# Kernel optimization log

Hardware: AMD Instinct MI355X
Metric: run time of the kernel (lower is better)

## Reference

```python
import jax, jax.numpy as jnp
import numpy as np

N = 50000        # nodes
E = 800000       # edges
D_IN = 128       # input feature dim
HID = 64         # hidden_dim
HEADS = 4
OUT = 2          # output_dim (fraud / not-fraud)
BN_EPS = 1e-5
NEG_SLOPE = 0.2  # PyG GATv2Conv default


def setup_inputs() -> dict:
    key = jax.random.key(0)
    ks = jax.random.split(key, 16)
    g = lambda k, shape, s=0.05: (jax.random.normal(k, shape, jnp.float32) * s)
    HC = HEADS * HID  # 256
    return {
        "x": jax.random.normal(ks[0], (N, D_IN), jnp.float32),
        "edge_index": jax.random.randint(ks[1], (2, E), 0, N),
        # input projection
        "W_in": g(ks[2], (D_IN, HID)), "b_in": jnp.zeros((HID,), jnp.float32),
        # GATv2 layer 0: HID -> HID, 4 heads (concat -> 256)
        "Wl0": g(ks[3], (HID, HC)), "Wr0": g(ks[4], (HID, HC)),
        "att0": g(ks[5], (HEADS, HID)), "bias0": jnp.zeros((HC,), jnp.float32),
        # GATv2 layer 1: 256 -> HID, 4 heads (concat -> 256)
        "Wl1": g(ks[6], (HC, HC)), "Wr1": g(ks[7], (HC, HC)),
        "att1": g(ks[8], (HEADS, HID)), "bias1": jnp.zeros((HC,), jnp.float32),
        # GATv2 layer 2: 256 -> OUT, 1 head
        "Wl2": g(ks[9], (HC, OUT)), "Wr2": g(ks[10], (HC, OUT)),
        "att2": g(ks[11], (1, OUT)), "bias2": jnp.zeros((OUT,), jnp.float32),
        # BatchNorm (eval mode: running stats) for the first num_layers-1 = 2 layers
        "bn_gamma": jnp.ones((2, HC), jnp.float32),
        "bn_beta": jnp.zeros((2, HC), jnp.float32),
        "bn_mean": jnp.zeros((2, HC), jnp.float32),
        "bn_var": jnp.ones((2, HC), jnp.float32),
    }


def _gatv2(h, src, dst, Wl, Wr, att, bias):
    """PyG GATv2Conv (concat=True, negative_slope=0.2). src->dst messages."""
    n = h.shape[0]
    heads, c = att.shape
    xl = (h @ Wl).reshape(n, heads, c)   # source transform
    xr = (h @ Wr).reshape(n, heads, c)   # target transform
    e = jax.nn.leaky_relu(xl[src] + xr[dst], NEG_SLOPE)       # [E, H, C]
    logits = jnp.einsum('ehc,hc->eh', e, att)                 # [E, H]
    # segment softmax over incoming edges of each destination node
    m = jax.ops.segment_max(logits, dst, num_segments=n)      # [N, H]
    ex = jnp.exp(logits - m[dst])
    denom = jax.ops.segment_sum(ex, dst, num_segments=n)
    alpha = ex / denom[dst]                                   # [E, H]
    out = jax.ops.segment_sum(xl[src] * alpha[..., None], dst, num_segments=n)
    return out.reshape(n, heads * c) + bias


def _bn_eval(h, gamma, beta, mean, var):
    return gamma * (h - mean) * jax.lax.rsqrt(var + BN_EPS) + beta


def reference(x, edge_index, W_in, b_in, Wl0, Wr0, att0, bias0,
              Wl1, Wr1, att1, bias1, Wl2, Wr2, att2, bias2,
              bn_gamma, bn_beta, bn_mean, bn_var):
    n = x.shape[0]
    loop = jnp.arange(n)
    src = jnp.concatenate([edge_index[0], loop])  # PyG add_self_loops=True
    dst = jnp.concatenate([edge_index[1], loop])

    h = jax.nn.relu(x @ W_in + b_in)              # dropout is identity in eval

    # layer 0 (no residual: 64 != 256)
    h = _gatv2(h, src, dst, Wl0, Wr0, att0, bias0)
    h = jax.nn.relu(_bn_eval(h, bn_gamma[0], bn_beta[0], bn_mean[0], bn_var[0]))

    # layer 1 (residual: 256 == 256)
    h_prev = h
    h = _gatv2(h, src, dst, Wl1, Wr1, att1, bias1)
    h = jax.nn.relu(_bn_eval(h, bn_gamma[1], bn_beta[1], bn_mean[1], bn_var[1]))
    h = h + h_prev

    # output layer, 1 head
    h = _gatv2(h, src, dst, Wl2, Wr2, att2, bias2)
    return jax.nn.log_softmax(h, axis=1)
```

## Files before the change

### kernel.cpp

```cpp
#include <hip/hip_runtime.h>
#include <hip/hip_bf16.h>
#include <math.h>


using h16     = _Float16;
using half2v  = __attribute__((ext_vector_type(2))) h16;
using half4v  = __attribute__((ext_vector_type(4))) h16;
using half8   = __attribute__((ext_vector_type(8))) h16;
using floatx2 = __attribute__((ext_vector_type(2))) float;
using floatx4 = __attribute__((ext_vector_type(4))) float;

__device__ __forceinline__ float lrelu(float x) { return x > 0.f ? x : 0.2f * x; }

__device__ __forceinline__ half2v shfl_xor_h2(half2v v, int mask) {
    float f = __builtin_bit_cast(float, v);
    f = __shfl_xor(f, mask, 64);
    return __builtin_bit_cast(half2v, f);
}

__global__ __launch_bounds__(256) void scan_blk(const int* __restrict__ deg,
                                                int* __restrict__ rowstart,
                                                int* __restrict__ bsum,
                                                int* __restrict__ bins, int N) {
    __shared__ int lhist[32];
    if (threadIdx.x < 32) lhist[threadIdx.x] = 0;
    __syncthreads();
    int t = blockIdx.x * 256 + threadIdx.x;
    int lane = threadIdx.x & 63, wid = threadIdx.x >> 6;
    int v = 0;
    if (t < N) {
        v = (deg[t] + 4) & ~3;
        atomicAdd(&lhist[min(v >> 2, 31)], 1);
    }
    int x = v;
#pragma unroll
    for (int off = 1; off < 64; off <<= 1) {
        int y = __shfl_up(x, off, 64);
        if (lane >= off) x += y;
    }
    __shared__ int wsum[4];
    if (lane == 63) wsum[wid] = x;
    __syncthreads();
    int add = 0;
#pragma unroll
    for (int w = 0; w < 4; ++w) if (w < wid) add += wsum[w];
    int incl = x + add;
    if (t < N) rowstart[t] = incl - v;
    if (threadIdx.x == 255) bsum[blockIdx.x] = incl;
    if (threadIdx.x < 32) {
        int c = lhist[threadIdx.x];
        if (c) atomicAdd(&bins[threadIdx.x], c);
    }
}

__global__ __launch_bounds__(256) void scan_off(int* __restrict__ bsum, int NB,
                                                const int* __restrict__ bins,
                                                int* __restrict__ bincur) {
    int t = threadIdx.x;
    int lane = t & 63, wid = t >> 6;
    int v = (t < NB) ? bsum[t] : 0;
    int x = v;
#pragma unroll
    for (int off = 1; off < 64; off <<= 1) {
        int y = __shfl_up(x, off, 64);
        if (lane >= off) x += y;
    }
    __shared__ int wsum[4];
    if (lane == 63) wsum[wid] = x;
    __syncthreads();
    int add = 0;
#pragma unroll
    for (int w = 0; w < 4; ++w) if (w < wid) add += wsum[w];
    if (t < NB) bsum[t] = x + add - v;
    if (t < 32) {
        int b = bins[t];
        int xb = b;
#pragma unroll
        for (int off2 = 1; off2 < 32; off2 <<= 1) {
            int y = __shfl_up(xb, off2, 64);
            if (t >= off2) xb += y;
        }
        bincur[t] = xb - b;
    }
}

__global__ __launch_bounds__(256) void add_off(
        const int* __restrict__ bsum, const int* __restrict__ deg,
        int* __restrict__ rowstart, int* __restrict__ cursor,
        int* __restrict__ csr_src,
        int* __restrict__ bincur, int* __restrict__ perm, int N) {
    __shared__ int lhist[32], lbase[32], lcur[32];
    if (threadIdx.x < 32) { lhist[threadIdx.x] = 0; lcur[threadIdx.x] = 0; }
    __syncthreads();
    int t = blockIdx.x * 256 + threadIdx.x;
    int b = 0;
    bool valid = t < N;
    if (valid) {
        int r = rowstart[t] + bsum[blockIdx.x];
        rowstart[t] = r;
        cursor[t] = r;
        int dg = deg[t];
        int npad = (dg + 4) & ~3;
        for (int k = dg; k < npad; ++k) csr_src[r + k] = t;
        b = min(npad >> 2, 31);
        atomicAdd(&lhist[b], 1);
    }
    __syncthreads();
    if (threadIdx.x < 32) {
        int c = lhist[threadIdx.x];
        lbase[threadIdx.x] = c ? atomicAdd(&bincur[threadIdx.x], c) : 0;
    }
    __syncthreads();
    if (valid) {
        int rank = atomicAdd(&lcur[b], 1);
        perm[lbase[b] + rank] = t;
    }
}

__device__ __forceinline__ void pack_one(const float* __restrict__ W,
                                         h16* __restrict__ Wp,
                                         int t, int K, int NC) {
    int j = t & 7;
    int l = (t >> 3) & 63;
    int rest = t >> 9;
    int NT = NC >> 4;
    int nt = rest % NT;
    int kc = rest / NT;
    int row = kc * 32 + (l >> 4) * 8 + j;
    int col = nt * 16 + (l & 15);
    Wp[t] = (h16)W[(size_t)row * NC + col];
}

__global__ void pack_all(const float* __restrict__ W_in,
                         const float* __restrict__ Wl0, const float* __restrict__ Wr0,
                         const float* __restrict__ Wl1, const float* __restrict__ Wr1,
                         h16* __restrict__ P_in,
                         h16* __restrict__ P_l0, h16* __restrict__ P_r0,
                         h16* __restrict__ P_l1, h16* __restrict__ P_r1,
                         const float4* __restrict__ x, half4v* __restrict__ xh, int n4,
                         const int* __restrict__ ei, int E, int* __restrict__ deg) {
    int t = blockIdx.x * blockDim.x + threadIdx.x;
    if (t < 8192)        pack_one(W_in, P_in, t, 128, 64);
    else if (t < 24576)  pack_one(Wl0, P_l0, t - 8192, 64, 256);
    else if (t < 40960)  pack_one(Wr0, P_r0, t - 24576, 64, 256);
    else if (t < 106496) pack_one(Wl1, P_l1, t - 40960, 256, 256);
    else if (t < 172032) pack_one(Wr1, P_r1, t - 106496, 256, 256);
    else if (t < 172032 + n4) {
        int u = t - 172032;
        float4 v = x[u];
        half4v o = { (h16)v.x, (h16)v.y, (h16)v.z, (h16)v.w };
        xh[u] = o;
    } else {
        int u = t - 172032 - n4;
        if (u < E) atomicAdd(&deg[ei[E + u]], 1);
    }
}

template<int KC, int NT, bool RELU>
__device__ __forceinline__ void gemm_body(const h16* __restrict__ Xh,
                                          const h16* __restrict__ Wp,
                                          const float* __restrict__ bias,
                                          h16* __restrict__ outp, int M, int bx) {
    constexpr int K = KC * 32;
    constexpr int ldo = NT * 16;
    constexpr int CHUNK8 = NT * 64;
    constexpr int PER_THR = CHUNK8 / 256;
    __shared__ half8 wbuf[2][CHUNK8];

    const half8* WG = (const half8*)Wp;
    const int tid = threadIdx.x;
    const int wid = tid >> 6, lane = tid & 63;
    const int quad = lane >> 4, li = lane & 15;
    const int r0 = bx * 64 + wid * 16;
    int arow = r0 + li; if (arow >= M) arow = M - 1;
    const half8* A8 = (const half8*)Xh + (size_t)arow * (K / 8) + quad;

    floatx4 acc[NT];
#pragma unroll
    for (int t = 0; t < NT; ++t) acc[t] = (floatx4){0.f, 0.f, 0.f, 0.f};

    half8 st[PER_THR];
#pragma unroll
    for (int i = 0; i < PER_THR; ++i) st[i] = WG[i * 256 + tid];
#pragma unroll
    for (int i = 0; i < PER_THR; ++i) wbuf[0][i * 256 + tid] = st[i];
    __syncthreads();

#pragma unroll
    for (int kc = 0; kc < KC; ++kc) {
        int cur = kc & 1;
        if (kc + 1 < KC) {
#pragma unroll
            for (int i = 0; i < PER_THR; ++i)
                st[i] = WG[(size_t)(kc + 1) * CHUNK8 + i * 256 + tid];
        }
        half8 a = A8[kc * 4];
#pragma unroll
        for (int nt = 0; nt < NT; ++nt) {
            half8 b = wbuf[cur][nt * 64 + lane];
            acc[nt] = __builtin_amdgcn_mfma_f32_16x16x32_f16(a, b, acc[nt], 0, 0, 0);
        }
        if (kc + 1 < KC) {
#pragma unroll
            for (int i = 0; i < PER_THR; ++i) wbuf[cur ^ 1][i * 256 + tid] = st[i];
        }
        __syncthreads();
    }

#pragma unroll
    for (int nt = 0; nt < NT; ++nt) {
#pragma unroll
        for (int reg = 0; reg < 4; ++reg) {
            int rr = r0 + quad * 4 + reg;
            if (rr >= M) continue;
            float v = acc[nt][reg];
            if (RELU) v = fmaxf(v + bias[nt * 16 + li], 0.f);
            outp[(size_t)rr * ldo + nt * 16 + li] = (h16)v;
        }
    }
}

template<int KC, int NT, bool RELU, bool DUAL>
__global__ __launch_bounds__(256) void gemm_lds(
        const h16* __restrict__ Xh,
        const h16* __restrict__ Wp0, const h16* __restrict__ Wp1,
        const float* __restrict__ bias,
        h16* __restrict__ out0, h16* __restrict__ out1, int M) {
    const h16* Wp = (DUAL && blockIdx.y) ? Wp1 : Wp0;
    h16* outp = (DUAL && blockIdx.y) ? out1 : out0;
    gemm_body<KC, NT, RELU>(Xh, Wp, bias, outp, M, blockIdx.x);
}

__global__ __launch_bounds__(256) void scatter_gemm0(
        const int* __restrict__ ei, int E,
        int* __restrict__ cursor, int* __restrict__ csr_src, int GS,
        const h16* __restrict__ xh, const h16* __restrict__ Wp_in,
        const float* __restrict__ b_in, h16* __restrict__ H0h, int M) {
    if ((int)blockIdx.x < GS) {
        int e = blockIdx.x * 256 + threadIdx.x;
        if (e < E) {
            int d = ei[E + e];
            int pos = atomicAdd(&cursor[d], 1);
            csr_src[pos] = ei[e];
        }
    } else {
        gemm_body<4, 4, true>(xh, Wp_in, b_in, H0h, M, blockIdx.x - GS);
    }
}

__global__ void attn4_bn(int N, const h16* __restrict__ XL,
                         const h16* __restrict__ XR,
                         const float* __restrict__ att,
                         const int* __restrict__ perm,
                         const int* __restrict__ rowstart, const int* __restrict__ deg,
                         const int* __restrict__ csr_src,
                         const float* __restrict__ gamma, const float* __restrict__ beta,
                         const float* __restrict__ mean, const float* __restrict__ var,
                         const float* __restrict__ bias, const h16* __restrict__ resid,
                         h16* __restrict__ outb) {
    int wv = blockIdx.x * (blockDim.x >> 6) + (threadIdx.x >> 6);
    if (wv * 4 >= N) return;
    int lane = threadIdx.x & 63;
    int sl   = lane & 15;
    int idx  = wv * 4 + (lane >> 4);
    bool dvalid = idx < N;
    int dh = perm[dvalid ? idx : (N - 1)];

    int start = rowstart[dh];
    int dg    = deg[dh];
    int nreal = dg + 1;
    int npad  = (dg + 4) & ~3;
    int m1    = max(npad, __shfl_xor(npad, 16, 64));
    int npmax = max(m1, __shfl_xor(m1, 32, 64));

    union H16 { uint4 u[2]; half2v h[8]; };
    H16 bv, wt;
    bv.u[0] = *(const uint4*)(XR + (size_t)dh * 256 + sl * 16);
    bv.u[1] = *(const uint4*)(XR + (size_t)dh * 256 + sl * 16 + 8);
    {
        const float* ar = att + sl * 16;
#pragma unroll
        for (int q = 0; q < 4; ++q) {
            float4 w = *(const float4*)(ar + q * 4);
            wt.h[2*q]   = half2v{(h16)w.x, (h16)w.y};
            wt.h[2*q+1] = half2v{(h16)w.z, (h16)w.w};
        }
    }
    const h16 k02 = (h16)0.2f;
    const uint4* XLv = (const uint4*)XL;

    auto ep = [&](const H16& x) -> h16 {
        half2v q{(h16)0, (h16)0};
#pragma unroll
        for (int j = 0; j < 8; ++j) {
            half2v e  = x.h[j] + bv.h[j];
            half2v lr = __builtin_elementwise_max(e, e * k02);
            q += lr * wt.h[j];
        }
        return q.x + q.y;
    };

    float l = 0.f;
    half2v acc[8];
#pragma unroll
    for (int j = 0; j < 8; ++j) acc[j] = half2v{(h16)0, (h16)0};

    int4 iv = *(const int4*)(csr_src + start);
    for (int i = 0; i < npmax; i += 4) {
        int4 cur = iv;
        if (i + 4 < npmax) {
            int nxt = min(i + 4, npad - 4);
            iv = *(const int4*)(csr_src + start + nxt);
        }
        H16 x0, x1, x2, x3;
        size_t a0 = (size_t)(unsigned)cur.x * 32 + sl * 2;
        size_t a1 = (size_t)(unsigned)cur.y * 32 + sl * 2;
        size_t a2 = (size_t)(unsigned)cur.z * 32 + sl * 2;
        size_t a3 = (size_t)(unsigned)cur.w * 32 + sl * 2;
        x0.u[0] = XLv[a0]; x0.u[1] = XLv[a0 + 1];
        x1.u[0] = XLv[a1]; x1.u[1] = XLv[a1 + 1];
        x2.u[0] = XLv[a2]; x2.u[1] = XLv[a2 + 1];
        x3.u[0] = XLv[a3]; x3.u[1] = XLv[a3 + 1];
        half2v p01 = { ep(x0), ep(x1) };
        half2v p23 = { ep(x2), ep(x3) };
#pragma unroll
        for (int s = 1; s < 4; s <<= 1) {
            p01 += shfl_xor_h2(p01, s);
            p23 += shfl_xor_h2(p23, s);
        }
        int rem = nreal - i;
        float e0 = (rem > 0) ? __expf((float)p01.x) : 0.f;
        float e1 = (rem > 1) ? __expf((float)p01.y) : 0.f;
        float e2 = (rem > 2) ? __expf((float)p23.x) : 0.f;
        float e3 = (rem > 3) ? __expf((float)p23.y) : 0.f;
        l += (e0 + e1) + (e2 + e3);
        h16 h0 = (h16)e0, h1 = (h16)e1, h2 = (h16)e2, h3 = (h16)e3;
        half2v eb0{h0,h0}, eb1{h1,h1}, eb2{h2,h2}, eb3{h3,h3};
#pragma unroll
        for (int j = 0; j < 8; ++j) {
            acc[j] += eb0 * x0.h[j];
            acc[j] += eb1 * x1.h[j];
            acc[j] += eb2 * x2.h[j];
            acc[j] += eb3 * x3.h[j];
        }
    }

    float inv = 1.f / l;
    float oc[16];
#pragma unroll
    for (int j = 0; j < 8; ++j) { oc[2*j] = (float)acc[j].x; oc[2*j+1] = (float)acc[j].y; }
    const float4* g4  = (const float4*)gamma;
    const float4* be4 = (const float4*)beta;
    const float4* mu4 = (const float4*)mean;
    const float4* va4 = (const float4*)var;
    const float4* bi4 = (const float4*)bias;
    float o[16];
#pragma unroll
    for (int q = 0; q < 4; ++q) {
        int ci = sl * 4 + q;
        float4 g  = g4[ci], bb = be4[ci], mu = mu4[ci];
        float4 va = va4[ci], bi = bi4[ci];
        float s0 = g.x * rsqrtf(va.x + 1e-5f);
        float s1 = g.y * rsqrtf(va.y + 1e-5f);
        float s2 = g.z * rsqrtf(va.z + 1e-5f);
        float s3 = g.w * rsqrtf(va.w + 1e-5f);
        o[q*4+0] = fmaxf(oc[q*4+0]*inv*s0 + (bi.x-mu.x)*s0 + bb.x, 0.f);
        o[q*4+1] = fmaxf(oc[q*4+1]*inv*s1 + (bi.y-mu.y)*s1 + bb.y, 0.f);
        o[q*4+2] = fmaxf(oc[q*4+2]*inv*s2 + (bi.z-mu.z)*s2 + bb.z, 0.f);
        o[q*4+3] = fmaxf(oc[q*4+3]*inv*s3 + (bi.w-mu.w)*s3 + bb.w, 0.f);
    }
    if (resid) {
        H16 rv;
        rv.u[0] = *(const uint4*)(resid + (size_t)dh * 256 + sl * 16);
        rv.u[1] = *(const uint4*)(resid + (size_t)dh * 256 + sl * 16 + 8);
#pragma unroll
        for (int j = 0; j < 8; ++j) {
            o[2*j]   += (float)rv.h[j].x;
            o[2*j+1] += (float)rv.h[j].y;
        }
    }
    if (dvalid) {
        H16 ov;
#pragma unroll
        for (int j = 0; j < 8; ++j) ov.h[j] = half2v{(h16)o[2*j], (h16)o[2*j+1]};
        *(uint4*)(outb + (size_t)dh * 256 + sl * 16)     = ov.u[0];
        *(uint4*)(outb + (size_t)dh * 256 + sl * 16 + 8) = ov.u[1];
    }
}

__global__ void gemm2_wave(const h16* __restrict__ X, const float* __restrict__ Wl,
                           const float* __restrict__ Wr, float* __restrict__ xl2,
                           float* __restrict__ xr2, int N) {
    int t = blockIdx.x * blockDim.x + threadIdx.x;
    int n = t >> 4;
    int sl = t & 15;
    if (n >= N) return;
    const half4v* Xr = (const half4v*)(X + (size_t)n * 256);
    const float4* Wl4 = (const float4*)Wl;
    const float4* Wr4 = (const float4*)Wr;
    float l0 = 0.f, l1 = 0.f, r0 = 0.f, r1 = 0.f;
#pragma unroll
    for (int j = 0; j < 4; ++j) {
        int idx = sl + j * 16;
        half4v xh = Xr[idx];
        float4 xv = { (float)xh.x, (float)xh.y, (float)xh.z, (float)xh.w };
        float4 wa = Wl4[idx * 2];
        float4 wb = Wl4[idx * 2 + 1];
        l0 += xv.x * wa.x + xv.y * wa.z + xv.z * wb.x + xv.w * wb.z;
        l1 += xv.x * wa.y + xv.y * wa.w + xv.z * wb.y + xv.w * wb.w;
        wa = Wr4[idx * 2]; wb = Wr4[idx * 2 + 1];
        r0 += xv.x * wa.x + xv.y * wa.z + xv.z * wb.x + xv.w * wb.z;
        r1 += xv.x * wa.y + xv.y * wa.w + xv.z * wb.y + xv.w * wb.w;
    }
#pragma unroll
    for (int off = 1; off < 16; off <<= 1) {
        l0 += __shfl_xor(l0, off, 64);
        l1 += __shfl_xor(l1, off, 64);
        r0 += __shfl_xor(r0, off, 64);
        r1 += __shfl_xor(r1, off, 64);
    }
    if (sl == 0) {
        xl2[n * 2] = l0; xl2[n * 2 + 1] = l1;
        xr2[n * 2] = r0; xr2[n * 2 + 1] = r1;
    }
}

__global__ void attn1_16(int N, const float* __restrict__ xl2, const float* __restrict__ xr2,
                         const float* __restrict__ att, const float* __restrict__ bias,
                         const int* __restrict__ rowstart, const int* __restrict__ deg,
                         const int* __restrict__ csr_src, float* __restrict__ out) {
    int t = blockIdx.x * blockDim.x + threadIdx.x;
    int d = t >> 4, sl = t & 15;
    if (d >= N) return;
    float a0 = att[0], a1 = att[1];
    float2 xr = ((const float2*)xr2)[d];
    float b0 = xr.x, b1 = xr.y;
    int st = rowstart[d];
    int nreal = deg[d] + 1;
    int npad  = (deg[d] + 4) & ~3;
    float l = 0.f, ac0 = 0.f, ac1 = 0.f;
    for (int i = sl; i < npad; i += 16) {
        int s = csr_src[st + i];
        float2 xv = ((const float2*)xl2)[s];
        float q = lrelu(xv.x + b0) * a0 + lrelu(xv.y + b1) * a1;
        float e = (i < nreal) ? __expf(q) : 0.f;
        l += e; ac0 += e * xv.x; ac1 += e * xv.y;
    }
#pragma unroll
    for (int off = 1; off < 16; off <<= 1) {
        l   += __shfl_xor(l, off, 64);
        ac0 += __shfl_xor(ac0, off, 64);
        ac1 += __shfl_xor(ac1, off, 64);
    }
    if (sl == 0) {
        float inv = 1.f / l;
        float v0 = ac0 * inv + bias[0];
        float v1 = ac1 * inv + bias[1];
        float mx = fmaxf(v0, v1);
        float lse = mx + logf(__expf(v0 - mx) + __expf(v1 - mx));
        out[d * 2] = v0 - lse;
        out[d * 2 + 1] = v1 - lse;
    }
}

extern "C" void kernel_launch(void* const* d_in, const int* in_sizes, int n_in,
                              void* d_out, int out_size, void* d_ws, size_t ws_size,
                              hipStream_t stream) {
    const float* x        = (const float*)d_in[0];
    const int*   ei       = (const int*)  d_in[1];
    const float* W_in     = (const float*)d_in[2];
    const float* b_in     = (const float*)d_in[3];
    const float* Wl0      = (const float*)d_in[4];
    const float* Wr0      = (const float*)d_in[5];
    const float* att0     = (const float*)d_in[6];
    const float* bias0    = (const float*)d_in[7];
    const float* Wl1      = (const float*)d_in[8];
    const float* Wr1      = (const float*)d_in[9];
    const float* att1     = (const float*)d_in[10];
    const float* bias1    = (const float*)d_in[11];
    const float* Wl2      = (const float*)d_in[12];
    const float* Wr2      = (const float*)d_in[13];
    const float* att2     = (const float*)d_in[14];
    const float* bias2    = (const float*)d_in[15];
    const float* bn_gamma = (const float*)d_in[16];
    const float* bn_beta  = (const float*)d_in[17];
    const float* bn_mean  = (const float*)d_in[18];
    const float* bn_var   = (const float*)d_in[19];

    const int N  = in_sizes[0] / 128;
    const int E  = in_sizes[1] / 2;
    const int NB = (N + 255) / 256;

    float* ws = (float*)d_ws;
    size_t off = 0;
    float* XL2  = ws + off; off += (size_t)N * 2;
    float* XR2  = ws + off; off += (size_t)N * 2;
    h16* Ah   = (h16*)(ws + off); off += (size_t)N * 128;
    h16* Bh   = (h16*)(ws + off); off += (size_t)N * 128;
    h16* Ch   = (h16*)(ws + off); off += (size_t)N * 128;
    h16* Dh   = (h16*)(ws + off); off += (size_t)N * 128;
    h16* H0h  = (h16*)(ws + off); off += (size_t)N * 32;
    h16* xh   = (h16*)(ws + off); off += (size_t)N * 64;
    h16* Wp_in = (h16*)(ws + off); off += 4096;
    h16* Wp_l0 = (h16*)(ws + off); off += 8192;
    h16* Wp_r0 = (h16*)(ws + off); off += 8192;
    h16* Wp_l1 = (h16*)(ws + off); off += 32768;
    h16* Wp_r1 = (h16*)(ws + off); off += 32768;
    int* ip = (int*)(ws + off);
    int* deg      = ip;              ip += N;
    int* bins     = ip;              ip += 32;
    int* bincur   = ip;              ip += 32;
    int* rowstart = ip;              ip += N;
    int* cursor   = ip;              ip += N;
    int* bsum     = ip;              ip += NB;
    int* perm     = ip;              ip += N;
    int* csr_src  = ip;              ip += E + 4 * N + 64;

    hipMemsetAsync(deg, 0, (size_t)(N + 32) * sizeof(int), stream);

    const int PACK_T = 172032 + N * 32 + E;
    pack_all<<<(PACK_T + 255) / 256, 256, 0, stream>>>(
        W_in, Wl0, Wr0, Wl1, Wr1, Wp_in, Wp_l0, Wp_r0, Wp_l1, Wp_r1,
        (const float4*)x, (half4v*)xh, N * 32, ei, E, deg);

    scan_blk<<<NB, 256, 0, stream>>>(deg, rowstart, bsum, bins, N);
    scan_off<<<1, 256, 0, stream>>>(bsum, NB, bins, bincur);
    add_off<<<NB, 256, 0, stream>>>(bsum, deg, rowstart, cursor, csr_src,
                                    bincur, perm, N);

    const int GBM = (N + 63) / 64;
    const int GS  = (E + 255) / 256;

    scatter_gemm0<<<GS + GBM, 256, 0, stream>>>(ei, E, cursor, csr_src, GS,
                                                xh, Wp_in, b_in, H0h, N);

    gemm_lds<2, 16, false, true><<<dim3(GBM, 2), 256, 0, stream>>>(
        H0h, Wp_l0, Wp_r0, nullptr, Ah, Bh, N);
    attn4_bn<<<(N + 15) / 16, 256, 0, stream>>>(N, Ah, Bh, att0, perm,
                                                rowstart, deg, csr_src,
                                                bn_gamma, bn_beta, bn_mean, bn_var,
                                                bias0, nullptr, Ch);

    gemm_lds<8, 16, false, true><<<dim3(GBM, 2), 256, 0, stream>>>(
        Ch, Wp_l1, Wp_r1, nullptr, Ah, Bh, N);
    attn4_bn<<<(N + 15) / 16, 256, 0, stream>>>(N, Ah, Bh, att1, perm,
                                                rowstart, deg, csr_src,
                                                bn_gamma + 256, bn_beta + 256, bn_mean + 256,
                                                bn_var + 256, bias1, Ch, Dh);

    gemm2_wave<<<(N * 16 + 255) / 256, 256, 0, stream>>>(Dh, Wl2, Wr2, XL2, XR2, N);
    attn1_16<<<(N * 16 + 255) / 256, 256, 0, stream>>>(N, XL2, XR2, att2, bias2,
                                                       rowstart, deg, csr_src, (float*)d_out);
}
```

Before: 418.3 us.

## Use 32 lanes per destination node in attention and pad scatter cursors

```diff
diff --git a/kernel.cpp b/kernel.cpp
--- a/kernel.cpp
+++ b/kernel.cpp
@@ -98,7 +98,7 @@
     if (valid) {
         int r = rowstart[t] + bsum[blockIdx.x];
         rowstart[t] = r;
-        cursor[t] = r;
+        cursor[(size_t)t * 16] = r;
         int dg = deg[t];
         int npad = (dg + 4) & ~3;
         for (int k = dg; k < npad; ++k) csr_src[r + k] = t;
@@ -240,7 +240,7 @@
         int e = blockIdx.x * 256 + threadIdx.x;
         if (e < E) {
             int d = ei[E + e];
-            int pos = atomicAdd(&cursor[d], 1);
+            int pos = atomicAdd(&cursor[(size_t)d * 16], 1);
             csr_src[pos] = ei[e];
         }
     } else {
@@ -259,10 +259,10 @@
                          const float* __restrict__ bias, const h16* __restrict__ resid,
                          h16* __restrict__ outb) {
     int wv = blockIdx.x * (blockDim.x >> 6) + (threadIdx.x >> 6);
-    if (wv * 4 >= N) return;
+    if (wv * 2 >= N) return;
     int lane = threadIdx.x & 63;
-    int sl   = lane & 15;
-    int idx  = wv * 4 + (lane >> 4);
+    int sl   = lane & 31;
+    int idx  = wv * 2 + (lane >> 5);
     bool dvalid = idx < N;
     int dh = perm[dvalid ? idx : (N - 1)];
 
@@ -270,29 +270,27 @@
     int dg    = deg[dh];
     int nreal = dg + 1;
     int npad  = (dg + 4) & ~3;
-    int m1    = max(npad, __shfl_xor(npad, 16, 64));
-    int npmax = max(m1, __shfl_xor(m1, 32, 64));
-
-    union H16 { uint4 u[2]; half2v h[8]; };
-    H16 bv, wt;
-    bv.u[0] = *(const uint4*)(XR + (size_t)dh * 256 + sl * 16);
-    bv.u[1] = *(const uint4*)(XR + (size_t)dh * 256 + sl * 16 + 8);
+    int npmax = max(npad, __shfl_xor(npad, 32, 64));
+
+    union H8 { uint4 u; half2v h[4]; };
+    H8 bv, wt;
+    bv.u = *(const uint4*)(XR + (size_t)dh * 256 + sl * 8);
     {
-        const float* ar = att + sl * 16;
-#pragma unroll
-        for (int q = 0; q < 4; ++q) {
-            float4 w = *(const float4*)(ar + q * 4);
-            wt.h[2*q]   = half2v{(h16)w.x, (h16)w.y};
-            wt.h[2*q+1] = half2v{(h16)w.z, (h16)w.w};
-        }
+        const float* ar = att + (sl >> 3) * 64 + (sl & 7) * 8;
+        float4 wa = *(const float4*)ar;
+        float4 wb = *(const float4*)(ar + 4);
+        wt.h[0] = half2v{(h16)wa.x, (h16)wa.y};
+        wt.h[1] = half2v{(h16)wa.z, (h16)wa.w};
+        wt.h[2] = half2v{(h16)wb.x, (h16)wb.y};
+        wt.h[3] = half2v{(h16)wb.z, (h16)wb.w};
     }
     const h16 k02 = (h16)0.2f;
-    const uint4* XLv = (const uint4*)XL;
-
-    auto ep = [&](const H16& x) -> h16 {
+    const uint2* XLv = (const uint2*)XL;
+
+    auto ep = [&](const H8& x) -> h16 {
         half2v q{(h16)0, (h16)0};
 #pragma unroll
-        for (int j = 0; j < 8; ++j) {
+        for (int j = 0; j < 4; ++j) {
             half2v e  = x.h[j] + bv.h[j];
             half2v lr = __builtin_elementwise_max(e, e * k02);
             q += lr * wt.h[j];
@@ -301,9 +299,8 @@
     };
 
     float l = 0.f;
-    half2v acc[8];
-#pragma unroll
-    for (int j = 0; j < 8; ++j) acc[j] = half2v{(h16)0, (h16)0};
+    half2v acc[4] = {half2v{(h16)0,(h16)0}, half2v{(h16)0,(h16)0},
+                     half2v{(h16)0,(h16)0}, half2v{(h16)0,(h16)0}};
 
     int4 iv = *(const int4*)(csr_src + start);
     for (int i = 0; i < npmax; i += 4) {
@@ -312,19 +309,29 @@
             int nxt = min(i + 4, npad - 4);
             iv = *(const int4*)(csr_src + start + nxt);
         }
-        H16 x0, x1, x2, x3;
-        size_t a0 = (size_t)(unsigned)cur.x * 32 + sl * 2;
-        size_t a1 = (size_t)(unsigned)cur.y * 32 + sl * 2;
-        size_t a2 = (size_t)(unsigned)cur.z * 32 + sl * 2;
-        size_t a3 = (size_t)(unsigned)cur.w * 32 + sl * 2;
-        x0.u[0] = XLv[a0]; x0.u[1] = XLv[a0 + 1];
-        x1.u[0] = XLv[a1]; x1.u[1] = XLv[a1 + 1];
-        x2.u[0] = XLv[a2]; x2.u[1] = XLv[a2 + 1];
-        x3.u[0] = XLv[a3]; x3.u[1] = XLv[a3 + 1];
-        half2v p01 = { ep(x0), ep(x1) };
-        half2v p23 = { ep(x2), ep(x3) };
-#pragma unroll
-        for (int s = 1; s < 4; s <<= 1) {
+        H8 x0, x1, x2, x3;
+        x0.u = __builtin_bit_cast(uint4, (uint2[2]){
+            XLv[(size_t)(unsigned)cur.x * 32 + sl], uint2{0,0}});
+        uint2 v0 = XLv[(size_t)(unsigned)cur.x * 32 + sl];
+        uint2 v1 = XLv[(size_t)(unsigned)cur.y * 32 + sl];
+        uint2 v2 = XLv[(size_t)(unsigned)cur.z * 32 + sl];
+        uint2 v3 = XLv[(size_t)(unsigned)cur.w * 32 + sl];
+        H8 y0, y1, y2, y3;
+        y0.u = uint4{v0.x, v0.y, 0, 0};
+        y1.u = uint4{v1.x, v1.y, 0, 0};
+        y2.u = uint4{v2.x, v2.y, 0, 0};
+        y3.u = uint4{v3.x, v3.y, 0, 0};
+        (void)y0; (void)y1; (void)y2; (void)y3; (void)x0;
+        const uint4* XL4 = (const uint4*)XL;
+        H8 z0, z1, z2, z3;
+        z0.u = XL4[(size_t)(unsigned)cur.x * 32 + sl];
+        z1.u = XL4[(size_t)(unsigned)cur.y * 32 + sl];
+        z2.u = XL4[(size_t)(unsigned)cur.z * 32 + sl];
+        z3.u = XL4[(size_t)(unsigned)cur.w * 32 + sl];
+        half2v p01 = { ep(z0), ep(z1) };
+        half2v p23 = { ep(z2), ep(z3) };
+#pragma unroll
+        for (int s = 1; s < 8; s <<= 1) {
             p01 += shfl_xor_h2(p01, s);
             p23 += shfl_xor_h2(p23, s);
         }
@@ -337,29 +344,28 @@
         h16 h0 = (h16)e0, h1 = (h16)e1, h2 = (h16)e2, h3 = (h16)e3;
         half2v eb0{h0,h0}, eb1{h1,h1}, eb2{h2,h2}, eb3{h3,h3};
 #pragma unroll
-        for (int j = 0; j < 8; ++j) {
-            acc[j] += eb0 * x0.h[j];
-            acc[j] += eb1 * x1.h[j];
-            acc[j] += eb2 * x2.h[j];
-            acc[j] += eb3 * x3.h[j];
+        for (int j = 0; j < 4; ++j) {
+            acc[j] += eb0 * z0.h[j];
+            acc[j] += eb1 * z1.h[j];
+            acc[j] += eb2 * z2.h[j];
+            acc[j] += eb3 * z3.h[j];
         }
     }
 
     float inv = 1.f / l;
-    float oc[16];
-#pragma unroll
-    for (int j = 0; j < 8; ++j) { oc[2*j] = (float)acc[j].x; oc[2*j+1] = (float)acc[j].y; }
+    float oc[8];
+#pragma unroll
+    for (int j = 0; j < 4; ++j) { oc[2*j] = (float)acc[j].x; oc[2*j+1] = (float)acc[j].y; }
     const float4* g4  = (const float4*)gamma;
     const float4* be4 = (const float4*)beta;
     const float4* mu4 = (const float4*)mean;
     const float4* va4 = (const float4*)var;
     const float4* bi4 = (const float4*)bias;
-    float o[16];
-#pragma unroll
-    for (int q = 0; q < 4; ++q) {
-        int ci = sl * 4 + q;
-        float4 g  = g4[ci], bb = be4[ci], mu = mu4[ci];
-        float4 va = va4[ci], bi = bi4[ci];
+    float o[8];
+#pragma unroll
+    for (int q = 0; q < 2; ++q) {
+        float4 g  = g4[sl*2+q],  bb = be4[sl*2+q], mu = mu4[sl*2+q];
+        float4 va = va4[sl*2+q], bi = bi4[sl*2+q];
         float s0 = g.x * rsqrtf(va.x + 1e-5f);
         float s1 = g.y * rsqrtf(va.y + 1e-5f);
         float s2 = g.z * rsqrtf(va.z + 1e-5f);
@@ -370,21 +376,18 @@
         o[q*4+3] = fmaxf(oc[q*4+3]*inv*s3 + (bi.w-mu.w)*s3 + bb.w, 0.f);
     }
     if (resid) {
-        H16 rv;
-        rv.u[0] = *(const uint4*)(resid + (size_t)dh * 256 + sl * 16);
-        rv.u[1] = *(const uint4*)(resid + (size_t)dh * 256 + sl * 16 + 8);
-#pragma unroll
-        for (int j = 0; j < 8; ++j) {
+        H8 rv; rv.u = *(const uint4*)(resid + (size_t)dh * 256 + sl * 8);
+#pragma unroll
+        for (int j = 0; j < 4; ++j) {
             o[2*j]   += (float)rv.h[j].x;
             o[2*j+1] += (float)rv.h[j].y;
         }
     }
     if (dvalid) {
-        H16 ov;
-#pragma unroll
-        for (int j = 0; j < 8; ++j) ov.h[j] = half2v{(h16)o[2*j], (h16)o[2*j+1]};
-        *(uint4*)(outb + (size_t)dh * 256 + sl * 16)     = ov.u[0];
-        *(uint4*)(outb + (size_t)dh * 256 + sl * 16 + 8) = ov.u[1];
+        H8 ov;
+#pragma unroll
+        for (int j = 0; j < 4; ++j) ov.h[j] = half2v{(h16)o[2*j], (h16)o[2*j+1]};
+        *(uint4*)(outb + (size_t)dh * 256 + sl * 8) = ov.u;
     }
 }
 
@@ -511,9 +514,9 @@
     int* bins     = ip;              ip += 32;
     int* bincur   = ip;              ip += 32;
     int* rowstart = ip;              ip += N;
-    int* cursor   = ip;              ip += N;
     int* bsum     = ip;              ip += NB;
     int* perm     = ip;              ip += N;
+    int* cursor   = ip;              ip += (size_t)N * 16;
     int* csr_src  = ip;              ip += E + 4 * N + 64;
 
     hipMemsetAsync(deg, 0, (size_t)(N + 32) * sizeof(int), stream);
@@ -536,17 +539,17 @@
 
     gemm_lds<2, 16, false, true><<<dim3(GBM, 2), 256, 0, stream>>>(
         H0h, Wp_l0, Wp_r0, nullptr, Ah, Bh, N);
-    attn4_bn<<<(N + 15) / 16, 256, 0, stream>>>(N, Ah, Bh, att0, perm,
-                                                rowstart, deg, csr_src,
-                                                bn_gamma, bn_beta, bn_mean, bn_var,
-                                                bias0, nullptr, Ch);
+    attn4_bn<<<(N + 7) / 8, 256, 0, stream>>>(N, Ah, Bh, att0, perm,
+                                              rowstart, deg, csr_src,
+                                              bn_gamma, bn_beta, bn_mean, bn_var,
+                                              bias0, nullptr, Ch);
 
     gemm_lds<8, 16, false, true><<<dim3(GBM, 2), 256, 0, stream>>>(
         Ch, Wp_l1, Wp_r1, nullptr, Ah, Bh, N);
-    attn4_bn<<<(N + 15) / 16, 256, 0, stream>>>(N, Ah, Bh, att1, perm,
-                                                rowstart, deg, csr_src,
-                                                bn_gamma + 256, bn_beta + 256, bn_mean + 256,
-                                                bn_var + 256, bias1, Ch, Dh);
+    attn4_bn<<<(N + 7) / 8, 256, 0, stream>>>(N, Ah, Bh, att1, perm,
+                                              rowstart, deg, csr_src,
+                                              bn_gamma + 256, bn_beta + 256, bn_mean + 256,
+                                              bn_var + 256, bias1, Ch, Dh);
 
     gemm2_wave<<<(N * 16 + 255) / 256, 256, 0, stream>>>(Dh, Wl2, Wr2, XL2, XR2, N);
     attn1_16<<<(N * 16 + 255) / 256, 256, 0, stream>>>(N, XL2, XR2, att2, bias2,
```

Measured after the change: 419.8 us. Within noise of the previous version (+0.3%).
